# Performance work log

Measured on AMD Instinct MI355X. Metric: run time of the kernel, lower is better.

## Reference

```python
import jax, jax.numpy as jnp
import numpy as np

N = 300000   # active voxels
K = 27       # 3^3 kernel offsets (kernel_size=3, D=3)
CIN = 64
COUT = 96
EPS = 1e-5   # MinkowskiBatchNorm default eps


def setup_inputs() -> dict:
    key = jax.random.key(0)
    ks = jax.random.split(key, 4)
    x = jax.random.normal(ks[0], (N, CIN), jnp.float32)
    nbrs = jax.random.randint(ks[1], (N, K), 0, N, jnp.int32)
    W1 = jax.random.normal(ks[2], (K, CIN, COUT), jnp.float32) * (1.0 / np.sqrt(K * CIN))
    W2 = jax.random.normal(ks[3], (K, COUT, COUT), jnp.float32) * (1.0 / np.sqrt(K * COUT))
    g1 = jnp.ones((COUT,), jnp.float32)
    b1 = jnp.zeros((COUT,), jnp.float32)
    g2 = jnp.ones((COUT,), jnp.float32)
    b2 = jnp.zeros((COUT,), jnp.float32)
    return {"x": x, "nbrs": nbrs, "W1": W1, "g1": g1, "b1": b1,
            "W2": W2, "g2": g2, "b2": b2}


def _sparse_conv(x, nbrs, W):
    # x: [N, Cin], nbrs: [N, K], W: [K, Cin, Cout]
    # Gather-GEMM-scatter with identical in/out coords (stride-1 3^D conv):
    # out[i] = sum_k x[nbrs[i,k]] @ W[k]. Scan over K to avoid the [N,K,Cin] blowup.
    acc0 = jnp.zeros((x.shape[0], W.shape[-1]), x.dtype)
    def step(acc, kw):
        nbr_k, W_k = kw
        return acc + x[nbr_k] @ W_k, None
    acc, _ = jax.lax.scan(step, acc0, (nbrs.T, W))
    return acc


def _bn_relu(h, gamma, beta):
    # training-mode batch norm over the point axis, then ReLU
    mu = jnp.mean(h, axis=0)
    var = jnp.var(h, axis=0)
    return jax.nn.relu((h - mu) * jax.lax.rsqrt(var + EPS) * gamma + beta)


def reference(x, nbrs, W1, g1, b1, W2, g2, b2):
    h = _bn_relu(_sparse_conv(x, nbrs, W1), g1, b1)
    return _bn_relu(_sparse_conv(h, nbrs, W2), g2, b2)
```

## Files before the change

### kernel.cpp

```cpp
#include <hip/hip_runtime.h>
#include <hip/hip_bf16.h>
#include <stdint.h>

#define N_VOX 300000
#define KNB   27
#define COUT  96
#define EPS   1e-5f
#define BM    256
#define NBLK  ((N_VOX + BM - 1) / BM)

typedef __attribute__((ext_vector_type(8))) short  short8;
typedef __attribute__((ext_vector_type(4))) float  f32x4;
typedef __attribute__((ext_vector_type(4))) float  float4v;
typedef __attribute__((ext_vector_type(4))) unsigned short ushort4v;

__device__ __forceinline__ unsigned short f2bf(float f) {
    uint32_t u = __float_as_uint(f);
    uint32_t r = (u + 0x7FFFu + ((u >> 16) & 1u)) >> 16;
    return (unsigned short)r;
}
__device__ __forceinline__ float bf2f(unsigned short b) {
    return __uint_as_float(((uint32_t)b) << 16);
}

__global__ void cast_x_kernel(const float4v* __restrict__ x, ushort4v* __restrict__ xb, int n4) {
    int i = blockIdx.x * blockDim.x + threadIdx.x;
    int stride = gridDim.x * blockDim.x;
    for (; i < n4; i += stride) {
        float4v v = x[i];
        ushort4v o;
        o.x = f2bf(v.x); o.y = f2bf(v.y); o.z = f2bf(v.z); o.w = f2bf(v.w);
        xb[i] = o;
    }
}

template <int S>
__global__ void cast_w_kernel(const float* __restrict__ W, unsigned short* __restrict__ Wt,
                              int total) {
    int idx = blockIdx.x * blockDim.x + threadIdx.x;
    if (idx >= total) return;
    int j    = idx & 7;
    int ual  = idx >> 3;
    int lane = ual & 63;
    int lo   = lane & 15;
    int hi   = lane >> 4;
    int rest = ual >> 6;
    int s    = rest % S;
    int cfk  = rest / S;
    int cf   = cfk % 6;
    int k    = cfk / 6;
    int cin  = s * 32 + hi * 8 + j;
    int cout = cf * 16 + lo;
    Wt[idx] = f2bf(W[(k * (S * 32) + cin) * COUT + cout]);
}

template <int CIN, bool F32OUT>
__launch_bounds__(512, 4)
__global__ void conv_kernel(const unsigned short* __restrict__ X,
                            const int* __restrict__ nbrs,
                            const unsigned short* __restrict__ Wt,
                            void* __restrict__ out,
                            float* __restrict__ partials) {
    constexpr int S      = CIN / 32;
    constexpr int BUNITS = 6 * S * 64;
    constexpr int CHUNKS = BUNITS / 64;
    constexpr int NSTG   = (CHUNKS + 7) / 8;

    __shared__ int nbr_s[BM * KNB];
    __shared__ __align__(16) unsigned short bbuf[2][BUNITS * 8];

    const int tid  = threadIdx.x;
    const int blk  = blockIdx.x;
    const int base = blk * BM;
    const int w    = tid >> 6;
    const int l    = tid & 63;
    const int lo   = l & 15;
    const int hi   = l >> 4;

    for (int i = tid; i < BM * KNB; i += 512) {
        int gi = base * KNB + i;
        nbr_s[i] = (gi < N_VOX * KNB) ? nbrs[gi] : 0;
    }

    f32x4 acc[2][6];
#pragma unroll
    for (int f = 0; f < 2; ++f)
#pragma unroll
        for (int cf = 0; cf < 6; ++cf)
            acc[f][cf] = (f32x4){0.f, 0.f, 0.f, 0.f};

    short8 a0[2][S], a1[2][S], stg[NSTG];

    auto stage_load = [&](int k) {
        const unsigned short* src = Wt + (size_t)k * (BUNITS * 8);
#pragma unroll
        for (int n = 0; n < NSTG; ++n) {
            int c = w + n * 8;
            if (c < CHUNKS)
                stg[n] = *(const short8*)(src + c * 512 + l * 8);
        }
    };
    auto stage_write = [&](unsigned short* buf) {
#pragma unroll
        for (int n = 0; n < NSTG; ++n) {
            int c = w + n * 8;
            if (c < CHUNKS)
                *(short8*)&buf[c * 512 + l * 8] = stg[n];
        }
    };
    auto loadA = [&](int k, short8 (&a)[2][S]) {
#pragma unroll
        for (int f = 0; f < 2; ++f) {
            int v   = w * 32 + f * 16 + lo;
            int row = nbr_s[v * KNB + k];
            const unsigned short* xp = X + (size_t)row * CIN + hi * 8;
#pragma unroll
            for (int s = 0; s < S; ++s)
                a[f][s] = *(const short8*)(xp + s * 32);
        }
    };
    auto mfmaP = [&](const unsigned short* buf, short8 (&a)[2][S]) {
#pragma unroll
        for (int cf = 0; cf < 6; ++cf)
#pragma unroll
            for (int s = 0; s < S; ++s) {
                short8 b = *(const short8*)&buf[((cf * S + s) * 64 + l) * 8];
                acc[0][cf] = __builtin_amdgcn_mfma_f32_16x16x32_bf16(a[0][s], b, acc[0][cf], 0, 0, 0);
                acc[1][cf] = __builtin_amdgcn_mfma_f32_16x16x32_bf16(a[1][s], b, acc[1][cf], 0, 0, 0);
            }
    };

    stage_load(0);
    __syncthreads();
    stage_write(bbuf[0]);
    loadA(0, a0);
    __syncthreads();

#pragma unroll 1
    for (int kk = 0; kk < KNB - 1; kk += 2) {
        stage_load(kk + 1);
        loadA(kk + 1, a1);
        mfmaP(bbuf[0], a0);
        stage_write(bbuf[1]);
        __syncthreads();
        stage_load(kk + 2);
        loadA(kk + 2, a0);
        mfmaP(bbuf[1], a1);
        stage_write(bbuf[0]);
        __syncthreads();
    }
    mfmaP(bbuf[0], a0);
    __syncthreads();

    float s_sum[6], s_sq[6];
#pragma unroll
    for (int cf = 0; cf < 6; ++cf) { s_sum[cf] = 0.f; s_sq[cf] = 0.f; }

#pragma unroll
    for (int f = 0; f < 2; ++f) {
        int m0 = base + w * 32 + f * 16 + hi * 4;
#pragma unroll
        for (int i = 0; i < 4; ++i) {
            int m = m0 + i;
            bool valid = (m < N_VOX);
#pragma unroll
            for (int cf = 0; cf < 6; ++cf) {
                float val = acc[f][cf][i];
                int col = cf * 16 + lo;
                if (valid) {
                    if (F32OUT) ((float*)out)[(size_t)m * COUT + col] = val;
                    else ((unsigned short*)out)[(size_t)m * COUT + col] = f2bf(val);
                    s_sum[cf] += val;
                    s_sq[cf]  += val * val;
                }
            }
        }
    }

    float* stat = (float*)bbuf;
#pragma unroll
    for (int cf = 0; cf < 6; ++cf) {
        float s = s_sum[cf], q = s_sq[cf];
        s += __shfl_xor(s, 16); q += __shfl_xor(q, 16);
        s += __shfl_xor(s, 32); q += __shfl_xor(q, 32);
        if (hi == 0) {
            stat[w * 192 + cf * 16 + lo]       = s;
            stat[w * 192 + COUT + cf * 16 + lo] = q;
        }
    }
    __syncthreads();
    if (tid < 2 * COUT) {
        float v = 0.f;
#pragma unroll
        for (int ww = 0; ww < 8; ++ww) v += stat[ww * 192 + tid];
        partials[blk * (2 * COUT) + tid] = v;
    }
}

__global__ void finalize_kernel(const float* __restrict__ partials, int nblk,
                                const float* __restrict__ gamma, const float* __restrict__ beta,
                                float* __restrict__ scale, float* __restrict__ bias) {
    int c = blockIdx.x;
    int tid = threadIdx.x;
    float s = 0.f, q = 0.f;
    for (int b = tid; b < nblk; b += 256) {
        s += partials[b * 192 + c];
        q += partials[b * 192 + 96 + c];
    }
    __shared__ float rs[4], rq[4];
#pragma unroll
    for (int m = 1; m <= 32; m <<= 1) { s += __shfl_xor(s, m); q += __shfl_xor(q, m); }
    int wid = tid >> 6, lane = tid & 63;
    if (lane == 0) { rs[wid] = s; rq[wid] = q; }
    __syncthreads();
    if (tid == 0) {
        s = rs[0] + rs[1] + rs[2] + rs[3];
        q = rq[0] + rq[1] + rq[2] + rq[3];
        float mu  = s / (float)N_VOX;
        float var = q / (float)N_VOX - mu * mu;
        float rsg = rsqrtf(var + EPS);
        float sc  = gamma[c] * rsg;
        scale[c] = sc;
        bias[c]  = beta[c] - mu * sc;
    }
}

__global__ void bnrelu_bf16_kernel(unsigned short* __restrict__ h,
                                   const float* __restrict__ scale,
                                   const float* __restrict__ bias, int total) {
    __shared__ float sc[COUT], bi[COUT];
    if (threadIdx.x < COUT) { sc[threadIdx.x] = scale[threadIdx.x]; bi[threadIdx.x] = bias[threadIdx.x]; }
    __syncthreads();
    int i = blockIdx.x * blockDim.x + threadIdx.x;
    int stride = gridDim.x * blockDim.x;
    for (; i < total; i += stride) {
        int c = i % COUT;
        float v = bf2f(h[i]) * sc[c] + bi[c];
        h[i] = f2bf(fmaxf(v, 0.f));
    }
}

__global__ void bnrelu_f32_kernel(float* __restrict__ h,
                                  const float* __restrict__ scale,
                                  const float* __restrict__ bias, int total) {
    __shared__ float sc[COUT], bi[COUT];
    if (threadIdx.x < COUT) { sc[threadIdx.x] = scale[threadIdx.x]; bi[threadIdx.x] = bias[threadIdx.x]; }
    __syncthreads();
    int i = blockIdx.x * blockDim.x + threadIdx.x;
    int stride = gridDim.x * blockDim.x;
    for (; i < total; i += stride) {
        int c = i % COUT;
        float v = h[i] * sc[c] + bi[c];
        h[i] = fmaxf(v, 0.f);
    }
}

extern "C" void kernel_launch(void* const* d_in, const int* in_sizes, int n_in,
                              void* d_out, int out_size, void* d_ws, size_t ws_size,
                              hipStream_t stream) {
    const float* x    = (const float*)d_in[0];
    const int*   nbrs = (const int*)  d_in[1];
    const float* W1   = (const float*)d_in[2];
    const float* g1   = (const float*)d_in[3];
    const float* b1   = (const float*)d_in[4];
    const float* W2   = (const float*)d_in[5];
    const float* g2   = (const float*)d_in[6];
    const float* b2   = (const float*)d_in[7];

    char* ws = (char*)d_ws;
    unsigned short* xb  = (unsigned short*)(ws);
    unsigned short* h0  = (unsigned short*)(ws + 38400000);
    unsigned short* w1t = (unsigned short*)(ws + 96000000);
    unsigned short* w2t = (unsigned short*)(ws + 96331776);
    float* p1    = (float*)(ws + 96829440);
    float* p2    = (float*)(ws + 97729536);
    float* sb    = (float*)(ws + 98629632);
    float* scale1 = sb;
    float* bias1  = sb + 96;
    float* scale2 = sb + 192;
    float* bias2  = sb + 288;

    cast_x_kernel<<<2048, 256, 0, stream>>>((const float4v*)x, (ushort4v*)xb, N_VOX * 64 / 4);
    {
        int tot1 = KNB * 64 * COUT;
        cast_w_kernel<2><<<(tot1 + 255) / 256, 256, 0, stream>>>(W1, w1t, tot1);
        int tot2 = KNB * 96 * COUT;
        cast_w_kernel<3><<<(tot2 + 255) / 256, 256, 0, stream>>>(W2, w2t, tot2);
    }

    conv_kernel<64, false><<<NBLK, 512, 0, stream>>>(xb, nbrs, w1t, h0, p1);

    finalize_kernel<<<96, 256, 0, stream>>>(p1, NBLK, g1, b1, scale1, bias1);
    bnrelu_bf16_kernel<<<2048, 256, 0, stream>>>(h0, scale1, bias1, N_VOX * COUT);

    conv_kernel<96, true><<<NBLK, 512, 0, stream>>>(h0, nbrs, w2t, d_out, p2);

    finalize_kernel<<<96, 256, 0, stream>>>(p2, NBLK, g2, b2, scale2, bias2);
    bnrelu_f32_kernel<<<2048, 256, 0, stream>>>((float*)d_out, scale2, bias2, N_VOX * COUT);
}
```

Measured before the change: 586.2 us.

## Halve conv tile rows, drop LDS neighbor staging, prefetch neighbor indices in registers

Shrinks the block tile from 256 to 128 voxels so each wave computes one 16-row fragment, which halves the accumulator and A-operand registers and raises launch bounds to 6 blocks per CU. The shared-memory neighbor table is removed; each lane loads its own neighbor indices from global memory one step ahead, and the barriers use an explicit lgkmcnt wait plus s_barrier. This is meant to raise occupancy and cut LDS use, but it doubles the weight staging traffic per voxel and adds more blocks. The p2 partials buffer is moved to alias the start of the workspace, where the bf16 copy of x lives; this assumes xb is no longer read by the time p2 is written.

```diff
diff --git a/kernel.cpp b/kernel.cpp
--- a/kernel.cpp
+++ b/kernel.cpp
@@ -6,7 +6,7 @@
 #define KNB   27
 #define COUT  96
 #define EPS   1e-5f
-#define BM    256
+#define BM    128
 #define NBLK  ((N_VOX + BM - 1) / BM)
 
 typedef __attribute__((ext_vector_type(8))) short  short8;
@@ -21,6 +21,12 @@
 }
 __device__ __forceinline__ float bf2f(unsigned short b) {
     return __uint_as_float(((uint32_t)b) << 16);
+}
+
+__device__ __forceinline__ void barrier_lgkm() {
+    asm volatile("s_waitcnt lgkmcnt(0)" ::: "memory");
+    __builtin_amdgcn_s_barrier();
+    asm volatile("" ::: "memory");
 }
 
 __global__ void cast_x_kernel(const float4v* __restrict__ x, ushort4v* __restrict__ xb, int n4) {
@@ -55,7 +61,7 @@
 }
 
 template <int CIN, bool F32OUT>
-__launch_bounds__(512, 4)
+__launch_bounds__(512, 6)
 __global__ void conv_kernel(const unsigned short* __restrict__ X,
                             const int* __restrict__ nbrs,
                             const unsigned short* __restrict__ Wt,
@@ -66,7 +72,6 @@
     constexpr int CHUNKS = BUNITS / 64;
     constexpr int NSTG   = (CHUNKS + 7) / 8;
 
-    __shared__ int nbr_s[BM * KNB];
     __shared__ __align__(16) unsigned short bbuf[2][BUNITS * 8];
 
     const int tid  = threadIdx.x;
@@ -77,19 +82,16 @@
     const int lo   = l & 15;
     const int hi   = l >> 4;
 
-    for (int i = tid; i < BM * KNB; i += 512) {
-        int gi = base * KNB + i;
-        nbr_s[i] = (gi < N_VOX * KNB) ? nbrs[gi] : 0;
-    }
-
-    f32x4 acc[2][6];
-#pragma unroll
-    for (int f = 0; f < 2; ++f)
-#pragma unroll
-        for (int cf = 0; cf < 6; ++cf)
-            acc[f][cf] = (f32x4){0.f, 0.f, 0.f, 0.f};
-
-    short8 a0[2][S], a1[2][S], stg[NSTG];
+    const int vrow  = base + w * 16 + lo;
+    const int vcl   = vrow < N_VOX ? vrow : 0;
+    const size_t nbase = (size_t)vcl * KNB;
+
+    f32x4 acc[6];
+#pragma unroll
+    for (int cf = 0; cf < 6; ++cf)
+        acc[cf] = (f32x4){0.f, 0.f, 0.f, 0.f};
+
+    short8 a0[S], a1[S], stg[NSTG];
 
     auto stage_load = [&](int k) {
         const unsigned short* src = Wt + (size_t)k * (BUNITS * 8);
@@ -108,46 +110,44 @@
                 *(short8*)&buf[c * 512 + l * 8] = stg[n];
         }
     };
-    auto loadA = [&](int k, short8 (&a)[2][S]) {
-#pragma unroll
-        for (int f = 0; f < 2; ++f) {
-            int v   = w * 32 + f * 16 + lo;
-            int row = nbr_s[v * KNB + k];
-            const unsigned short* xp = X + (size_t)row * CIN + hi * 8;
-#pragma unroll
-            for (int s = 0; s < S; ++s)
-                a[f][s] = *(const short8*)(xp + s * 32);
-        }
-    };
-    auto mfmaP = [&](const unsigned short* buf, short8 (&a)[2][S]) {
+    auto loadA = [&](int row, short8 (&a)[S]) {
+        const unsigned short* xp = X + (size_t)row * CIN + hi * 8;
+#pragma unroll
+        for (int s = 0; s < S; ++s)
+            a[s] = *(const short8*)(xp + s * 32);
+    };
+    auto mfmaP = [&](const unsigned short* buf, short8 (&a)[S]) {
 #pragma unroll
         for (int cf = 0; cf < 6; ++cf)
 #pragma unroll
             for (int s = 0; s < S; ++s) {
                 short8 b = *(const short8*)&buf[((cf * S + s) * 64 + l) * 8];
-                acc[0][cf] = __builtin_amdgcn_mfma_f32_16x16x32_bf16(a[0][s], b, acc[0][cf], 0, 0, 0);
-                acc[1][cf] = __builtin_amdgcn_mfma_f32_16x16x32_bf16(a[1][s], b, acc[1][cf], 0, 0, 0);
+                acc[cf] = __builtin_amdgcn_mfma_f32_16x16x32_bf16(a[s], b, acc[cf], 0, 0, 0);
             }
     };
 
+    int nbA = nbrs[nbase + 0];
+    int nbB = nbrs[nbase + 1];
     stage_load(0);
-    __syncthreads();
+    loadA(nbA, a0);
     stage_write(bbuf[0]);
-    loadA(0, a0);
+    nbA = nbrs[nbase + 2];
     __syncthreads();
 
 #pragma unroll 1
     for (int kk = 0; kk < KNB - 1; kk += 2) {
         stage_load(kk + 1);
-        loadA(kk + 1, a1);
+        loadA(nbB, a1);
+        nbB = nbrs[nbase + (kk + 3 < KNB ? kk + 3 : KNB - 1)];
         mfmaP(bbuf[0], a0);
         stage_write(bbuf[1]);
-        __syncthreads();
+        barrier_lgkm();
         stage_load(kk + 2);
-        loadA(kk + 2, a0);
+        loadA(nbA, a0);
+        nbA = nbrs[nbase + (kk + 4 < KNB ? kk + 4 : KNB - 1)];
         mfmaP(bbuf[1], a1);
         stage_write(bbuf[0]);
-        __syncthreads();
+        barrier_lgkm();
     }
     mfmaP(bbuf[0], a0);
     __syncthreads();
@@ -156,23 +156,20 @@
 #pragma unroll
     for (int cf = 0; cf < 6; ++cf) { s_sum[cf] = 0.f; s_sq[cf] = 0.f; }
 
-#pragma unroll
-    for (int f = 0; f < 2; ++f) {
-        int m0 = base + w * 32 + f * 16 + hi * 4;
-#pragma unroll
-        for (int i = 0; i < 4; ++i) {
-            int m = m0 + i;
-            bool valid = (m < N_VOX);
-#pragma unroll
-            for (int cf = 0; cf < 6; ++cf) {
-                float val = acc[f][cf][i];
-                int col = cf * 16 + lo;
-                if (valid) {
-                    if (F32OUT) ((float*)out)[(size_t)m * COUT + col] = val;
-                    else ((unsigned short*)out)[(size_t)m * COUT + col] = f2bf(val);
-                    s_sum[cf] += val;
-                    s_sq[cf]  += val * val;
-                }
+    const int m0 = base + w * 16 + hi * 4;
+#pragma unroll
+    for (int i = 0; i < 4; ++i) {
+        int m = m0 + i;
+        bool valid = (m < N_VOX);
+#pragma unroll
+        for (int cf = 0; cf < 6; ++cf) {
+            float val = acc[cf][i];
+            int col = cf * 16 + lo;
+            if (valid) {
+                if (F32OUT) ((float*)out)[(size_t)m * COUT + col] = val;
+                else ((unsigned short*)out)[(size_t)m * COUT + col] = f2bf(val);
+                s_sum[cf] += val;
+                s_sq[cf]  += val * val;
             }
         }
     }
@@ -184,7 +181,7 @@
         s += __shfl_xor(s, 16); q += __shfl_xor(q, 16);
         s += __shfl_xor(s, 32); q += __shfl_xor(q, 32);
         if (hi == 0) {
-            stat[w * 192 + cf * 16 + lo]       = s;
+            stat[w * 192 + cf * 16 + lo]        = s;
             stat[w * 192 + COUT + cf * 16 + lo] = q;
         }
     }
@@ -269,11 +266,11 @@
 
     char* ws = (char*)d_ws;
     unsigned short* xb  = (unsigned short*)(ws);
+    float*          p2  = (float*)(ws);
     unsigned short* h0  = (unsigned short*)(ws + 38400000);
     unsigned short* w1t = (unsigned short*)(ws + 96000000);
     unsigned short* w2t = (unsigned short*)(ws + 96331776);
     float* p1    = (float*)(ws + 96829440);
-    float* p2    = (float*)(ws + 97729536);
     float* sb    = (float*)(ws + 98629632);
     float* scale1 = sb;
     float* bias1  = sb + 96;
```

Result: slower. 638.4 us (+8.9%).

## Fuse first BN-ReLU into second conv gather and stream neighbor indices

Applied to the files above, without the earlier changes.

The first BN+ReLU is applied on the fly to gathered bf16 rows inside the second conv, which removes the standalone in-place pass over h0. Neighbor indices are now prefetched per tap from global memory into registers instead of being staged in a large LDS array, and barriers wait only on LDS counters. When the workspace is large enough, the second conv writes a bf16 intermediate that a vectorized kernel expands to the fp32 output with BN+ReLU, which cuts intermediate traffic. The cost is extra ALU work per MFMA for the fused affine transform, recomputed once for every one of the 27 taps, and an extra rounding of the final conv output to bf16.

```diff
diff --git a/kernel.cpp b/kernel.cpp
--- a/kernel.cpp
+++ b/kernel.cpp
@@ -21,6 +21,12 @@
 }
 __device__ __forceinline__ float bf2f(unsigned short b) {
     return __uint_as_float(((uint32_t)b) << 16);
+}
+
+__device__ __forceinline__ void barrier_lgkm() {
+    asm volatile("s_waitcnt lgkmcnt(0)" ::: "memory");
+    __builtin_amdgcn_s_barrier();
+    asm volatile("" ::: "memory");
 }
 
 __global__ void cast_x_kernel(const float4v* __restrict__ x, ushort4v* __restrict__ xb, int n4) {
@@ -54,11 +60,12 @@
     Wt[idx] = f2bf(W[(k * (S * 32) + cin) * COUT + cout]);
 }
 
-template <int CIN, bool F32OUT>
+template <int CIN, bool FUSE_IN, bool OUT_BF16>
 __launch_bounds__(512, 4)
 __global__ void conv_kernel(const unsigned short* __restrict__ X,
                             const int* __restrict__ nbrs,
                             const unsigned short* __restrict__ Wt,
+                            const float* __restrict__ scbi_in,
                             void* __restrict__ out,
                             float* __restrict__ partials) {
     constexpr int S      = CIN / 32;
@@ -66,8 +73,8 @@
     constexpr int CHUNKS = BUNITS / 64;
     constexpr int NSTG   = (CHUNKS + 7) / 8;
 
-    __shared__ int nbr_s[BM * KNB];
     __shared__ __align__(16) unsigned short bbuf[2][BUNITS * 8];
+    __shared__ __align__(16) float scbi_s[2 * CIN];
 
     const int tid  = threadIdx.x;
     const int blk  = blockIdx.x;
@@ -77,9 +84,15 @@
     const int lo   = l & 15;
     const int hi   = l >> 4;
 
-    for (int i = tid; i < BM * KNB; i += 512) {
-        int gi = base * KNB + i;
-        nbr_s[i] = (gi < N_VOX * KNB) ? nbrs[gi] : 0;
+    if (FUSE_IN) {
+        if (tid < 2 * CIN) scbi_s[tid] = scbi_in[tid];
+    }
+
+    size_t nbase[2];
+#pragma unroll
+    for (int f = 0; f < 2; ++f) {
+        int vr = base + w * 32 + f * 16 + lo;
+        nbase[f] = (size_t)(vr < N_VOX ? vr : 0) * KNB;
     }
 
     f32x4 acc[2][6];
@@ -90,6 +103,7 @@
             acc[f][cf] = (f32x4){0.f, 0.f, 0.f, 0.f};
 
     short8 a0[2][S], a1[2][S], stg[NSTG];
+    int nbA[2], nbB[2];
 
     auto stage_load = [&](int k) {
         const unsigned short* src = Wt + (size_t)k * (BUNITS * 8);
@@ -108,46 +122,75 @@
                 *(short8*)&buf[c * 512 + l * 8] = stg[n];
         }
     };
-    auto loadA = [&](int k, short8 (&a)[2][S]) {
+    auto loadA = [&](const int (&row)[2], short8 (&a)[2][S]) {
 #pragma unroll
         for (int f = 0; f < 2; ++f) {
-            int v   = w * 32 + f * 16 + lo;
-            int row = nbr_s[v * KNB + k];
-            const unsigned short* xp = X + (size_t)row * CIN + hi * 8;
+            const unsigned short* xp = X + (size_t)row[f] * CIN + hi * 8;
 #pragma unroll
             for (int s = 0; s < S; ++s)
                 a[f][s] = *(const short8*)(xp + s * 32);
         }
     };
+    auto loadNbr = [&](int t, int (&nb)[2]) {
+        int tc = t < KNB ? t : KNB - 1;
+#pragma unroll
+        for (int f = 0; f < 2; ++f) nb[f] = nbrs[nbase[f] + tc];
+    };
     auto mfmaP = [&](const unsigned short* buf, short8 (&a)[2][S]) {
 #pragma unroll
-        for (int cf = 0; cf < 6; ++cf)
-#pragma unroll
-            for (int s = 0; s < S; ++s) {
+        for (int s = 0; s < S; ++s) {
+            short8 av[2];
+            if (FUSE_IN) {
+                const float4v* scp = (const float4v*)&scbi_s[s * 32 + hi * 8];
+                const float4v* bip = (const float4v*)&scbi_s[CIN + s * 32 + hi * 8];
+                float4v sc0 = scp[0], sc1 = scp[1];
+                float4v bi0 = bip[0], bi1 = bip[1];
+#pragma unroll
+                for (int f = 0; f < 2; ++f) {
+                    short8 r = a[f][s], t;
+#pragma unroll
+                    for (int j = 0; j < 4; ++j) {
+                        float v0 = fmaxf(bf2f((unsigned short)r[j])     * sc0[j] + bi0[j], 0.f);
+                        float v1 = fmaxf(bf2f((unsigned short)r[j + 4]) * sc1[j] + bi1[j], 0.f);
+                        t[j]     = (short)f2bf(v0);
+                        t[j + 4] = (short)f2bf(v1);
+                    }
+                    av[f] = t;
+                }
+            } else {
+                av[0] = a[0][s]; av[1] = a[1][s];
+            }
+#pragma unroll
+            for (int cf = 0; cf < 6; ++cf) {
                 short8 b = *(const short8*)&buf[((cf * S + s) * 64 + l) * 8];
-                acc[0][cf] = __builtin_amdgcn_mfma_f32_16x16x32_bf16(a[0][s], b, acc[0][cf], 0, 0, 0);
-                acc[1][cf] = __builtin_amdgcn_mfma_f32_16x16x32_bf16(a[1][s], b, acc[1][cf], 0, 0, 0);
+                acc[0][cf] = __builtin_amdgcn_mfma_f32_16x16x32_bf16(av[0], b, acc[0][cf], 0, 0, 0);
+                acc[1][cf] = __builtin_amdgcn_mfma_f32_16x16x32_bf16(av[1], b, acc[1][cf], 0, 0, 0);
             }
-    };
-
+        }
+    };
+
+    loadNbr(0, nbA);
+    loadNbr(1, nbB);
     stage_load(0);
-    __syncthreads();
+    loadA(nbA, a0);
     stage_write(bbuf[0]);
-    loadA(0, a0);
+    loadNbr(2, nbA);
     __syncthreads();
 
 #pragma unroll 1
     for (int kk = 0; kk < KNB - 1; kk += 2) {
         stage_load(kk + 1);
-        loadA(kk + 1, a1);
+        loadA(nbB, a1);
+        loadNbr(kk + 3, nbB);
         mfmaP(bbuf[0], a0);
         stage_write(bbuf[1]);
-        __syncthreads();
+        barrier_lgkm();
         stage_load(kk + 2);
-        loadA(kk + 2, a0);
+        loadA(nbA, a0);
+        loadNbr(kk + 4, nbA);
         mfmaP(bbuf[1], a1);
         stage_write(bbuf[0]);
-        __syncthreads();
+        barrier_lgkm();
     }
     mfmaP(bbuf[0], a0);
     __syncthreads();
@@ -168,8 +211,8 @@
                 float val = acc[f][cf][i];
                 int col = cf * 16 + lo;
                 if (valid) {
-                    if (F32OUT) ((float*)out)[(size_t)m * COUT + col] = val;
-                    else ((unsigned short*)out)[(size_t)m * COUT + col] = f2bf(val);
+                    if (OUT_BF16) ((unsigned short*)out)[(size_t)m * COUT + col] = f2bf(val);
+                    else          ((float*)out)[(size_t)m * COUT + col] = val;
                     s_sum[cf] += val;
                     s_sq[cf]  += val * val;
                 }
@@ -184,7 +227,7 @@
         s += __shfl_xor(s, 16); q += __shfl_xor(q, 16);
         s += __shfl_xor(s, 32); q += __shfl_xor(q, 32);
         if (hi == 0) {
-            stat[w * 192 + cf * 16 + lo]       = s;
+            stat[w * 192 + cf * 16 + lo]        = s;
             stat[w * 192 + COUT + cf * 16 + lo] = q;
         }
     }
@@ -225,18 +268,27 @@
     }
 }
 
-__global__ void bnrelu_bf16_kernel(unsigned short* __restrict__ h,
-                                   const float* __restrict__ scale,
-                                   const float* __restrict__ bias, int total) {
+__global__ void bnrelu_bf16_to_f32_kernel(const unsigned short* __restrict__ y,
+                                          const float* __restrict__ scale,
+                                          const float* __restrict__ bias,
+                                          float* __restrict__ out, int n8) {
     __shared__ float sc[COUT], bi[COUT];
     if (threadIdx.x < COUT) { sc[threadIdx.x] = scale[threadIdx.x]; bi[threadIdx.x] = bias[threadIdx.x]; }
     __syncthreads();
     int i = blockIdx.x * blockDim.x + threadIdx.x;
     int stride = gridDim.x * blockDim.x;
-    for (; i < total; i += stride) {
-        int c = i % COUT;
-        float v = bf2f(h[i]) * sc[c] + bi[c];
-        h[i] = f2bf(fmaxf(v, 0.f));
+    for (; i < n8; i += stride) {
+        int e  = i * 8;
+        int c0 = e % COUT;
+        short8 v = *(const short8*)(y + e);
+        float4v o0, o1;
+#pragma unroll
+        for (int j = 0; j < 4; ++j) {
+            o0[j] = fmaxf(bf2f((unsigned short)v[j])     * sc[c0 + j]     + bi[c0 + j], 0.f);
+            o1[j] = fmaxf(bf2f((unsigned short)v[j + 4]) * sc[c0 + j + 4] + bi[c0 + j + 4], 0.f);
+        }
+        *(float4v*)(out + e)     = o0;
+        *(float4v*)(out + e + 4) = o1;
     }
 }
 
@@ -269,16 +321,18 @@
 
     char* ws = (char*)d_ws;
     unsigned short* xb  = (unsigned short*)(ws);
+    float*          p2  = (float*)(ws);
     unsigned short* h0  = (unsigned short*)(ws + 38400000);
     unsigned short* w1t = (unsigned short*)(ws + 96000000);
     unsigned short* w2t = (unsigned short*)(ws + 96331776);
     float* p1    = (float*)(ws + 96829440);
-    float* p2    = (float*)(ws + 97729536);
     float* sb    = (float*)(ws + 98629632);
-    float* scale1 = sb;
-    float* bias1  = sb + 96;
+    float* scbi1  = sb;
     float* scale2 = sb + 192;
     float* bias2  = sb + 288;
+    unsigned short* yraw = (unsigned short*)(ws + 98632704);
+
+    const bool use_yraw = (ws_size >= (size_t)98632704 + 57600000);
 
     cast_x_kernel<<<2048, 256, 0, stream>>>((const float4v*)x, (ushort4v*)xb, N_VOX * 64 / 4);
     {
@@ -288,13 +342,18 @@
         cast_w_kernel<3><<<(tot2 + 255) / 256, 256, 0, stream>>>(W2, w2t, tot2);
     }
 
-    conv_kernel<64, false><<<NBLK, 512, 0, stream>>>(xb, nbrs, w1t, h0, p1);
-
-    finalize_kernel<<<96, 256, 0, stream>>>(p1, NBLK, g1, b1, scale1, bias1);
-    bnrelu_bf16_kernel<<<2048, 256, 0, stream>>>(h0, scale1, bias1, N_VOX * COUT);
-
-    conv_kernel<96, true><<<NBLK, 512, 0, stream>>>(h0, nbrs, w2t, d_out, p2);
-
-    finalize_kernel<<<96, 256, 0, stream>>>(p2, NBLK, g2, b2, scale2, bias2);
-    bnrelu_f32_kernel<<<2048, 256, 0, stream>>>((float*)d_out, scale2, bias2, N_VOX * COUT);
-}
+    conv_kernel<64, false, true><<<NBLK, 512, 0, stream>>>(xb, nbrs, w1t, nullptr, h0, p1);
+
+    finalize_kernel<<<96, 256, 0, stream>>>(p1, NBLK, g1, b1, scbi1, scbi1 + 96);
+
+    if (use_yraw) {
+        conv_kernel<96, true, true><<<NBLK, 512, 0, stream>>>(h0, nbrs, w2t, scbi1, yraw, p2);
+        finalize_kernel<<<96, 256, 0, stream>>>(p2, NBLK, g2, b2, scale2, bias2);
+        bnrelu_bf16_to_f32_kernel<<<8192, 256, 0, stream>>>(yraw, scale2, bias2,
+                                                            (float*)d_out, N_VOX * COUT / 8);
+    } else {
+        conv_kernel<96, true, false><<<NBLK, 512, 0, stream>>>(h0, nbrs, w2t, scbi1, d_out, p2);
+        finalize_kernel<<<96, 256, 0, stream>>>(p2, NBLK, g2, b2, scale2, bias2);
+        bnrelu_f32_kernel<<<2048, 256, 0, stream>>>((float*)d_out, scale2, bias2, N_VOX * COUT);
+    }
+}
```

After: 825.6 us. 1.41x slower.
